# Performance work log

Hardware: AMD Instinct MI355X
Metric: run time of the kernel (lower is better)

Reference implementation:

```python
import jax, jax.numpy as jnp
import numpy as np

B, F, H, M, T = 4096, 256, 256, 3, 30
IN0 = 2 + F  # GRU layer-0 input: concat(current_pos[2], context[F])


def setup_inputs() -> dict:
    key = jax.random.key(0)
    ks = jax.random.split(key, 15)
    s = 0.05
    rn = lambda k, shp: jax.random.normal(k, shp, jnp.float32) * s
    return dict(
        context=jax.random.normal(ks[0], (B, F), jnp.float32),
        mp_w1=rn(ks[1], (64, F)), mp_b1=rn(ks[2], (64,)),
        mp_w2=rn(ks[3], (M, 64)), mp_b2=rn(ks[4], (M,)),
        w_ih0=rn(ks[5], (M, 3 * H, IN0)), w_hh0=rn(ks[6], (M, 3 * H, H)),
        b_ih0=rn(ks[7], (M, 3 * H)), b_hh0=rn(ks[8], (M, 3 * H)),
        w_ih1=rn(ks[9], (M, 3 * H, H)), w_hh1=rn(ks[10], (M, 3 * H, H)),
        b_ih1=rn(ks[11], (M, 3 * H)), b_hh1=rn(ks[12], (M, 3 * H)),
        out_w=rn(ks[13], (M, 2, H)), out_b=rn(ks[14], (M, 2)),
        num_future_steps=T,
    )


def _gru_cell(x, h, w_ih, w_hh, b_ih, b_hh):
    # PyTorch GRU cell, gate order (r, z, n)
    gx = x @ w_ih.T + b_ih  # (B, 3H)
    gh = h @ w_hh.T + b_hh  # (B, 3H)
    xr, xz, xn = jnp.split(gx, 3, axis=-1)
    hr, hz, hn = jnp.split(gh, 3, axis=-1)
    r = jax.nn.sigmoid(xr + hr)
    z = jax.nn.sigmoid(xz + hz)
    n = jnp.tanh(xn + r * hn)
    return (1.0 - z) * n + z * h


def reference(context, mp_w1, mp_b1, mp_w2, mp_b2,
              w_ih0, w_hh0, b_ih0, b_hh0,
              w_ih1, w_hh1, b_ih1, b_hh1,
              out_w, out_b, num_future_steps):
    mode_logits = jax.nn.relu(context @ mp_w1.T + mp_b1) @ mp_w2.T + mp_b2
    mode_probs = jax.nn.softmax(mode_logits, axis=-1)  # (B, M)

    def decode_mode(wi0, wh0, bi0, bh0, wi1, wh1, bi1, bh1, ow, ob):
        def step(carry, _):
            h0, h1, pos = carry
            x = jnp.concatenate([pos, context], axis=-1)  # (B, 2+F)
            h0n = _gru_cell(x, h0, wi0, wh0, bi0, bh0)
            h1n = _gru_cell(h0n, h1, wi1, wh1, bi1, bh1)
            delta = h1n @ ow.T + ob  # (B, 2)
            return (h0n, h1n, delta), delta

        pos0 = jnp.zeros((context.shape[0], 2), context.dtype)
        # hidden = context.unsqueeze(0).repeat(2,1,1): both layers init to context
        (_, _, _), deltas = jax.lax.scan(step, (context, context, pos0), None,
                                          length=num_future_steps)
        # deltas: (T, B, 2) -> (B, T, 2), cumulative sum over time
        return jnp.cumsum(deltas.transpose(1, 0, 2), axis=1)

    trajs = jax.vmap(decode_mode)(w_ih0, w_hh0, b_ih0, b_hh0,
                                  w_ih1, w_hh1, b_ih1, b_hh1,
                                  out_w, out_b)  # (M, B, T, 2)
    trajectories = trajs.transpose(1, 0, 2, 3)  # (B, M, T, 2)
    return trajectories, mode_probs
```

## Files before the change

kernel.cpp:

```cpp
#include <hip/hip_runtime.h>


typedef __attribute__((ext_vector_type(8))) short bf16x8;
typedef __attribute__((ext_vector_type(4))) float f32x4;
typedef __fp16 f16x2 __attribute__((ext_vector_type(2)));

__device__ __forceinline__ short f2bf(float f) {
    unsigned u = __builtin_bit_cast(unsigned, f);
    unsigned r = (u + 0x7fffu + ((u >> 16) & 1u)) >> 16;
    return (short)r;
}
__device__ __forceinline__ float bf2f(short s) {
    unsigned u = ((unsigned)(unsigned short)s) << 16;
    return __builtin_bit_cast(float, u);
}
__device__ __forceinline__ unsigned pkh2(float a, float b) {
    f16x2 v = __builtin_amdgcn_cvt_pkrtz(a, b);
    return __builtin_bit_cast(unsigned, v);
}
__device__ __forceinline__ float uph(unsigned u, int hi) {
    f16x2 v = __builtin_bit_cast(f16x2, u);
    return (float)(hi ? v[1] : v[0]);
}
__device__ __forceinline__ float fast_sigmoid(float x) {
    x = fminf(fmaxf(x, -30.f), 30.f);
    float e = __builtin_amdgcn_exp2f(x * -1.442695041f);
    return __builtin_amdgcn_rcpf(1.f + e);
}
__device__ __forceinline__ float fast_tanh(float x) {
    x = fminf(fmaxf(x, -15.f), 15.f);
    float e = __builtin_amdgcn_exp2f(x * -2.885390082f);
    return (1.f - e) * __builtin_amdgcn_rcpf(1.f + e);
}

__global__ void prep_kernel(const float* __restrict__ w_ih0,
                            const float* __restrict__ w_hh0,
                            const float* __restrict__ w_ih1,
                            const float* __restrict__ w_hh1,
                            short* __restrict__ ws) {
    int bid = blockIdx.x;
    int L = threadIdx.x;
    const float* src;
    int srcRowLen, colBase, m, w, ks, t;
    if (bid < 1152) {
        int idx = bid, mw = idx / 48, blk = idx % 48;
        m = mw / 8; w = mw % 8;
        if (blk < 32) { ks = blk >> 2; t = blk & 3; }
        else { int q = blk - 32; ks = q >> 1; t = 4 + (q & 1); }
        src = w_hh0 + (size_t)m * 768 * 256; srcRowLen = 256; colBase = 0;
    } else if (bid < 3456) {
        int idx = bid - 1152, mw = idx / 96, blk = idx % 96;
        m = mw / 8; w = mw % 8;
        int half;
        if (blk < 64) { half = blk >> 5; ks = (blk >> 2) & 7; t = blk & 3; }
        else { int q = blk - 64; half = q >> 4; ks = (q >> 1) & 7; t = 4 + (q & 1); }
        src = (half ? w_hh1 : w_ih1) + (size_t)m * 768 * 256;
        srcRowLen = 256; colBase = 0;
    } else {
        int idx = bid - 3456, mw = idx / 48, blk = idx % 48;
        m = mw / 8; w = mw % 8; ks = blk / 6; t = blk % 6;
        src = w_ih0 + (size_t)m * 768 * 258; srcRowLen = 258; colBase = 2;
    }
    int row = (t >> 1) * 256 + 32 * w + (t & 1) * 16 + (L & 15);
    int col0 = colBase + ks * 32 + (L >> 4) * 8;
    short* dst = ws + (size_t)bid * 512 + L * 8;
    const float* s = src + (size_t)row * srcRowLen + col0;
#pragma unroll
    for (int j = 0; j < 8; ++j) dst[j] = f2bf(s[j]);
}

__global__ __launch_bounds__(256) void modeprobs_kernel(
    const float* __restrict__ ctx, const float* __restrict__ w1,
    const float* __restrict__ b1, const float* __restrict__ w2,
    const float* __restrict__ b2, float* __restrict__ out,
    long probs_off) {
    __shared__ float w1s[64 * 256];
    int tid = threadIdx.x;
    int j = tid & 63;
    int rsub = tid >> 6;
#pragma unroll
    for (int i = 0; i < 64; ++i) w1s[tid + i * 256] = w1[tid + i * 256];
    float b1v = b1[j];
    float w2v0 = w2[j], w2v1 = w2[64 + j], w2v2 = w2[128 + j];
    float b20 = b2[0], b21 = b2[1], b22 = b2[2];
    __syncthreads();
    for (int c = 0; c < 16; ++c) {
        int brow = blockIdx.x * 64 + c * 4 + rsub;
        const float* crow = ctx + (size_t)brow * 256;
        float accv = b1v;
#pragma unroll 8
        for (int k = 0; k < 256; ++k) {
            int kk = (k + j) & 255;
            accv += w1s[j * 256 + kk] * crow[kk];
        }
        float h = fmaxf(accv, 0.f);
        float l0 = h * w2v0, l1 = h * w2v1, l2 = h * w2v2;
#pragma unroll
        for (int s = 1; s < 64; s <<= 1) {
            l0 += __shfl_xor(l0, s);
            l1 += __shfl_xor(l1, s);
            l2 += __shfl_xor(l2, s);
        }
        if (j == 0) {
            l0 += b20; l1 += b21; l2 += b22;
            float mx = fmaxf(l0, fmaxf(l1, l2));
            float e0 = __builtin_amdgcn_exp2f((l0 - mx) * 1.442695041f);
            float e1 = __builtin_amdgcn_exp2f((l1 - mx) * 1.442695041f);
            float e2 = __builtin_amdgcn_exp2f((l2 - mx) * 1.442695041f);
            float inv = 1.f / (e0 + e1 + e2);
            out[probs_off + (size_t)brow * 3 + 0] = e0 * inv;
            out[probs_off + (size_t)brow * 3 + 1] = e1 * inv;
            out[probs_off + (size_t)brow * 3 + 2] = e2 * inv;
        }
    }
}

__global__ __launch_bounds__(512, 2) void decoder_kernel(
    const float* __restrict__ context,
    const float* __restrict__ w_ih0_f,
    const float* __restrict__ b_ih0, const float* __restrict__ b_hh0,
    const float* __restrict__ b_ih1, const float* __restrict__ b_hh1,
    const float* __restrict__ out_w, const float* __restrict__ out_b,
    const short* __restrict__ ws, float* __restrict__ out,
    const int* __restrict__ pT, int ntiles) {
    __shared__ short ctxS[64 * 264];
    __shared__ short h0s[64 * 264];
    __shared__ short h1s[64 * 264];
    __shared__ float posD[128];
    __shared__ float owl[512];
    __shared__ float cwp0[768], cwp1[768];
    __shared__ float cbA[512];
    __shared__ float cbXn[256];
    __shared__ float cbh0n[256];
    __shared__ float cb1A[512];
    __shared__ float cb1X[256];
    __shared__ float cb1H[256];

    const int bid = blockIdx.x;
    const int xcd = bid & 7, slot = bid >> 3;
    int mode, xl, nx;
    if (xcd < 3)      { mode = 0; xl = xcd;     nx = 3; }
    else if (xcd < 6) { mode = 1; xl = xcd - 3; nx = 3; }
    else              { mode = 2; xl = xcd - 6; nx = 2; }
    const int g = slot * nx + xl;
    if (g >= ntiles) return;
    const int m = mode;
    const int b0 = g * 64;

    const int T = *pT;
    const int tid = threadIdx.x;
    const int lane = tid & 63, w = tid >> 6;
    const int lr = lane & 15, quad = lane >> 4;

    if (tid < 128) posD[tid] = 0.f;
    owl[tid] = out_w[m * 512 + tid];
    if (tid < 512) {
        cbA[tid] = b_ih0[m * 768 + tid] + b_hh0[m * 768 + tid];
        cb1A[tid] = b_ih1[m * 768 + tid] + b_hh1[m * 768 + tid];
    }
    if (tid < 256) {
        cbXn[tid] = b_ih0[m * 768 + 512 + tid];
        cbh0n[tid] = b_hh0[m * 768 + 512 + tid];
        cb1X[tid] = b_ih1[m * 768 + 512 + tid];
        cb1H[tid] = b_hh1[m * 768 + 512 + tid];
    }
    for (int c = tid; c < 768; c += 512) {
        cwp0[c] = w_ih0_f[((size_t)m * 768 + c) * 258 + 0];
        cwp1[c] = w_ih0_f[((size_t)m * 768 + c) * 258 + 1];
    }
#pragma unroll
    for (int i = 0; i < 32; ++i) {
        int idx = tid + i * 512;
        int r = idx >> 8, k = idx & 255;
        short v = f2bf(context[(size_t)(b0 + r) * 256 + k]);
        ctxS[r * 264 + k] = v;
        h0s[r * 264 + k] = v;
        h1s[r * 264 + k] = v;
    }
    const float ob0v = out_b[m * 2 + 0], ob1v = out_b[m * 2 + 1];

    const short* p0w = ws + ((size_t)(m * 8 + w) * 48) * 512 + lane * 8;
    const short* p1w = ws + (size_t)1152 * 512 + ((size_t)(m * 8 + w) * 96) * 512 + lane * 8;
    const short* pcw = ws + (size_t)3456 * 512 + ((size_t)(m * 8 + w) * 48) * 512 + lane * 8;

    const int cA = 32 * w + lr;
    const int cB = 32 * w + 16 + lr;

    __syncthreads();

    float cum0 = 0.f, cum1 = 0.f;

    for (int st = 0; st < T; ++st) {
        unsigned rp[2][4][2], zp[2][4][2];

        {
            f32x4 arz[4][4];
#pragma unroll
            for (int rt = 0; rt < 4; ++rt)
#pragma unroll
                for (int r = 0; r < 4; ++r) {
                    int row = rt * 16 + quad * 4 + r;
                    float px = posD[row * 2], py = posD[row * 2 + 1];
#pragma unroll
                    for (int t = 0; t < 4; ++t) {
                        int c = (t >> 1) * 256 + ((t & 1) ? cB : cA);
                        arz[t][rt][r] = cbA[c] + px * cwp0[c] + py * cwp1[c];
                    }
                }
            const short* bpc = pcw;
            const short* bp0 = p0w;
#pragma unroll 1
            for (int ks = 0; ks < 8; ++ks) {
                bf16x8 ac[4], ah[4];
#pragma unroll
                for (int rt = 0; rt < 4; ++rt) {
                    ac[rt] = *reinterpret_cast<const bf16x8*>(
                        ctxS + (rt * 16 + lr) * 264 + ks * 32 + quad * 8);
                    ah[rt] = *reinterpret_cast<const bf16x8*>(
                        h0s + (rt * 16 + lr) * 264 + ks * 32 + quad * 8);
                }
#pragma unroll
                for (int t = 0; t < 4; ++t) {
                    bf16x8 b = *reinterpret_cast<const bf16x8*>(bpc + t * 512);
#pragma unroll
                    for (int rt = 0; rt < 4; ++rt)
                        arz[t][rt] = __builtin_amdgcn_mfma_f32_16x16x32_bf16(
                            ac[rt], b, arz[t][rt], 0, 0, 0);
                }
#pragma unroll
                for (int t = 0; t < 4; ++t) {
                    bf16x8 b = *reinterpret_cast<const bf16x8*>(bp0 + t * 512);
#pragma unroll
                    for (int rt = 0; rt < 4; ++rt)
                        arz[t][rt] = __builtin_amdgcn_mfma_f32_16x16x32_bf16(
                            ah[rt], b, arz[t][rt], 0, 0, 0);
                }
                bpc += 6 * 512;
                bp0 += 4 * 512;
            }
#pragma unroll
            for (int nt = 0; nt < 2; ++nt)
#pragma unroll
                for (int rt = 0; rt < 4; ++rt) {
                    rp[nt][rt][0] = pkh2(fast_sigmoid(arz[nt][rt][0]),
                                         fast_sigmoid(arz[nt][rt][1]));
                    rp[nt][rt][1] = pkh2(fast_sigmoid(arz[nt][rt][2]),
                                         fast_sigmoid(arz[nt][rt][3]));
                    zp[nt][rt][0] = pkh2(fast_sigmoid(arz[2 + nt][rt][0]),
                                         fast_sigmoid(arz[2 + nt][rt][1]));
                    zp[nt][rt][1] = pkh2(fast_sigmoid(arz[2 + nt][rt][2]),
                                         fast_sigmoid(arz[2 + nt][rt][3]));
                }
        }
        {
            f32x4 axn[2][4], ahn[2][4];
#pragma unroll
            for (int rt = 0; rt < 4; ++rt)
#pragma unroll
                for (int r = 0; r < 4; ++r) {
                    int row = rt * 16 + quad * 4 + r;
                    float px = posD[row * 2], py = posD[row * 2 + 1];
#pragma unroll
                    for (int nt = 0; nt < 2; ++nt) {
                        int cn = nt ? cB : cA;
                        axn[nt][rt][r] = cbXn[cn] + px * cwp0[512 + cn] +
                                         py * cwp1[512 + cn];
                        ahn[nt][rt][r] = cbh0n[cn];
                    }
                }
            const short* bpc = pcw + 4 * 512;
            const short* bp0 = p0w + 32 * 512;
#pragma unroll 1
            for (int ks = 0; ks < 8; ++ks) {
                bf16x8 ac[4], ah[4];
#pragma unroll
                for (int rt = 0; rt < 4; ++rt) {
                    ac[rt] = *reinterpret_cast<const bf16x8*>(
                        ctxS + (rt * 16 + lr) * 264 + ks * 32 + quad * 8);
                    ah[rt] = *reinterpret_cast<const bf16x8*>(
                        h0s + (rt * 16 + lr) * 264 + ks * 32 + quad * 8);
                }
#pragma unroll
                for (int nt = 0; nt < 2; ++nt) {
                    bf16x8 b = *reinterpret_cast<const bf16x8*>(bpc + nt * 512);
#pragma unroll
                    for (int rt = 0; rt < 4; ++rt)
                        axn[nt][rt] = __builtin_amdgcn_mfma_f32_16x16x32_bf16(
                            ac[rt], b, axn[nt][rt], 0, 0, 0);
                }
#pragma unroll
                for (int nt = 0; nt < 2; ++nt) {
                    bf16x8 b = *reinterpret_cast<const bf16x8*>(bp0 + nt * 512);
#pragma unroll
                    for (int rt = 0; rt < 4; ++rt)
                        ahn[nt][rt] = __builtin_amdgcn_mfma_f32_16x16x32_bf16(
                            ah[rt], b, ahn[nt][rt], 0, 0, 0);
                }
                bpc += 6 * 512;
                bp0 += 2 * 512;
            }
            __syncthreads();
#pragma unroll
            for (int nt = 0; nt < 2; ++nt) {
                int col = nt ? cB : cA;
#pragma unroll
                for (int rt = 0; rt < 4; ++rt)
#pragma unroll
                    for (int r = 0; r < 4; ++r) {
                        int row = rt * 16 + quad * 4 + r;
                        float rr = uph(rp[nt][rt][r >> 1], r & 1);
                        float zz = uph(zp[nt][rt][r >> 1], r & 1);
                        float nn =
                            fast_tanh(axn[nt][rt][r] + rr * ahn[nt][rt][r]);
                        float hold = bf2f(h0s[row * 264 + col]);
                        h0s[row * 264 + col] = f2bf((1.f - zz) * nn + zz * hold);
                    }
            }
        }
        __syncthreads();

        {
            f32x4 arz[4][4];
#pragma unroll
            for (int rt = 0; rt < 4; ++rt)
#pragma unroll
                for (int r = 0; r < 4; ++r)
#pragma unroll
                    for (int t = 0; t < 4; ++t) {
                        int c = (t >> 1) * 256 + ((t & 1) ? cB : cA);
                        arz[t][rt][r] = cb1A[c];
                    }
            const short* bq0 = p1w;
            const short* bq1 = p1w + 32 * 512;
#pragma unroll 1
            for (int ks = 0; ks < 8; ++ks) {
                bf16x8 a0[4], a1[4];
#pragma unroll
                for (int rt = 0; rt < 4; ++rt) {
                    a0[rt] = *reinterpret_cast<const bf16x8*>(
                        h0s + (rt * 16 + lr) * 264 + ks * 32 + quad * 8);
                    a1[rt] = *reinterpret_cast<const bf16x8*>(
                        h1s + (rt * 16 + lr) * 264 + ks * 32 + quad * 8);
                }
#pragma unroll
                for (int t = 0; t < 4; ++t) {
                    bf16x8 b = *reinterpret_cast<const bf16x8*>(bq0 + t * 512);
#pragma unroll
                    for (int rt = 0; rt < 4; ++rt)
                        arz[t][rt] = __builtin_amdgcn_mfma_f32_16x16x32_bf16(
                            a0[rt], b, arz[t][rt], 0, 0, 0);
                }
#pragma unroll
                for (int t = 0; t < 4; ++t) {
                    bf16x8 b = *reinterpret_cast<const bf16x8*>(bq1 + t * 512);
#pragma unroll
                    for (int rt = 0; rt < 4; ++rt)
                        arz[t][rt] = __builtin_amdgcn_mfma_f32_16x16x32_bf16(
                            a1[rt], b, arz[t][rt], 0, 0, 0);
                }
                bq0 += 4 * 512;
                bq1 += 4 * 512;
            }
#pragma unroll
            for (int nt = 0; nt < 2; ++nt)
#pragma unroll
                for (int rt = 0; rt < 4; ++rt) {
                    rp[nt][rt][0] = pkh2(fast_sigmoid(arz[nt][rt][0]),
                                         fast_sigmoid(arz[nt][rt][1]));
                    rp[nt][rt][1] = pkh2(fast_sigmoid(arz[nt][rt][2]),
                                         fast_sigmoid(arz[nt][rt][3]));
                    zp[nt][rt][0] = pkh2(fast_sigmoid(arz[2 + nt][rt][0]),
                                         fast_sigmoid(arz[2 + nt][rt][1]));
                    zp[nt][rt][1] = pkh2(fast_sigmoid(arz[2 + nt][rt][2]),
                                         fast_sigmoid(arz[2 + nt][rt][3]));
                }
        }
        {
            f32x4 axn[2][4], ahn[2][4];
#pragma unroll
            for (int rt = 0; rt < 4; ++rt)
#pragma unroll
                for (int r = 0; r < 4; ++r)
#pragma unroll
                    for (int nt = 0; nt < 2; ++nt) {
                        int cn = nt ? cB : cA;
                        axn[nt][rt][r] = cb1X[cn];
                        ahn[nt][rt][r] = cb1H[cn];
                    }
            const short* bx = p1w + 64 * 512;
            const short* bh = p1w + 80 * 512;
#pragma unroll 1
            for (int ks = 0; ks < 8; ++ks) {
                bf16x8 a0[4], a1[4];
#pragma unroll
                for (int rt = 0; rt < 4; ++rt) {
                    a0[rt] = *reinterpret_cast<const bf16x8*>(
                        h0s + (rt * 16 + lr) * 264 + ks * 32 + quad * 8);
                    a1[rt] = *reinterpret_cast<const bf16x8*>(
                        h1s + (rt * 16 + lr) * 264 + ks * 32 + quad * 8);
                }
#pragma unroll
                for (int nt = 0; nt < 2; ++nt) {
                    bf16x8 b = *reinterpret_cast<const bf16x8*>(bx + nt * 512);
#pragma unroll
                    for (int rt = 0; rt < 4; ++rt)
                        axn[nt][rt] = __builtin_amdgcn_mfma_f32_16x16x32_bf16(
                            a0[rt], b, axn[nt][rt], 0, 0, 0);
                }
#pragma unroll
                for (int nt = 0; nt < 2; ++nt) {
                    bf16x8 b = *reinterpret_cast<const bf16x8*>(bh + nt * 512);
#pragma unroll
                    for (int rt = 0; rt < 4; ++rt)
                        ahn[nt][rt] = __builtin_amdgcn_mfma_f32_16x16x32_bf16(
                            a1[rt], b, ahn[nt][rt], 0, 0, 0);
                }
                bx += 2 * 512;
                bh += 2 * 512;
            }
            __syncthreads();
#pragma unroll
            for (int nt = 0; nt < 2; ++nt) {
                int col = nt ? cB : cA;
#pragma unroll
                for (int rt = 0; rt < 4; ++rt)
#pragma unroll
                    for (int r = 0; r < 4; ++r) {
                        int row = rt * 16 + quad * 4 + r;
                        float rr = uph(rp[nt][rt][r >> 1], r & 1);
                        float zz = uph(zp[nt][rt][r >> 1], r & 1);
                        float nn =
                            fast_tanh(axn[nt][rt][r] + rr * ahn[nt][rt][r]);
                        float hold = bf2f(h1s[row * 264 + col]);
                        h1s[row * 264 + col] = f2bf((1.f - zz) * nn + zz * hold);
                    }
            }
        }
        __syncthreads();

        {
            int brow = tid >> 3, p = tid & 7;
            float d0 = 0.f, d1 = 0.f;
#pragma unroll
            for (int j = 0; j < 4; ++j) {
                int cb = ((p + brow) & 7) * 8 + j * 64;
                bf16x8 hv8 = *reinterpret_cast<const bf16x8*>(h1s + brow * 264 + cb);
#pragma unroll
                for (int i = 0; i < 8; ++i) {
                    float hv = bf2f(hv8[i]);
                    d0 += hv * owl[cb + i];
                    d1 += hv * owl[256 + cb + i];
                }
            }
            d0 += __shfl_xor(d0, 1); d0 += __shfl_xor(d0, 2); d0 += __shfl_xor(d0, 4);
            d1 += __shfl_xor(d1, 1); d1 += __shfl_xor(d1, 2); d1 += __shfl_xor(d1, 4);
            d0 += ob0v;
            d1 += ob1v;
            if (p == 0) {
                cum0 += d0;
                cum1 += d1;
                size_t o = (((size_t)(b0 + brow) * 3 + m) * (size_t)T + st) * 2;
                out[o] = cum0;
                out[o + 1] = cum1;
                posD[brow * 2] = d0;
                posD[brow * 2 + 1] = d1;
            }
        }
        __syncthreads();
    }
}

extern "C" void kernel_launch(void* const* d_in, const int* in_sizes, int n_in,
                              void* d_out, int out_size, void* d_ws, size_t ws_size,
                              hipStream_t stream) {
    const float* context = (const float*)d_in[0];
    const float* mp_w1 = (const float*)d_in[1];
    const float* mp_b1 = (const float*)d_in[2];
    const float* mp_w2 = (const float*)d_in[3];
    const float* mp_b2 = (const float*)d_in[4];
    const float* w_ih0 = (const float*)d_in[5];
    const float* w_hh0 = (const float*)d_in[6];
    const float* b_ih0 = (const float*)d_in[7];
    const float* b_hh0 = (const float*)d_in[8];
    const float* w_ih1 = (const float*)d_in[9];
    const float* w_hh1 = (const float*)d_in[10];
    const float* b_ih1 = (const float*)d_in[11];
    const float* b_hh1 = (const float*)d_in[12];
    const float* out_w = (const float*)d_in[13];
    const float* out_b = (const float*)d_in[14];
    const int* pT = (const int*)d_in[15];
    float* out = (float*)d_out;
    short* ws = (short*)d_ws;

    const int B = in_sizes[0] / 256;
    const int ntiles = B / 64;
    const long probs_off = (long)out_size - (long)B * 3;

    prep_kernel<<<4608, 64, 0, stream>>>(w_ih0, w_hh0, w_ih1, w_hh1, ws);
    modeprobs_kernel<<<B / 64, 256, 0, stream>>>(context, mp_w1, mp_b1, mp_w2,
                                                 mp_b2, out, probs_off);
    const int nslots = (ntiles + 1) / 2;
    decoder_kernel<<<8 * nslots, 512, 0, stream>>>(
        context, w_ih0, b_ih0, b_hh0, b_ih1, b_hh1, out_w, out_b, ws, out, pT,
        ntiles);
}
```

Measured before the change: 1.045 ms.

## Hoist time-invariant context projection out of GRU step loop into AGPRs

The layer-0 input projection of the constant context (W_ih0 times context plus biases) is now computed once before the time loop and stored as packed bf16 in accumulator registers. Each step reads it back instead of redoing the context MFMAs, which removes about 40% of layer-0 matrix work per step and the ctxS shared buffer. The cost is extra register pressure from 48 AGPRs, which may hurt occupancy under the 512x2 launch bounds. Rounding the precomputed projection to bf16 also adds some precision loss.

```diff
diff --git a/kernel.cpp b/kernel.cpp
--- a/kernel.cpp
+++ b/kernel.cpp
@@ -14,6 +14,12 @@
     unsigned u = ((unsigned)(unsigned short)s) << 16;
     return __builtin_bit_cast(float, u);
 }
+__device__ __forceinline__ unsigned pk2(float a, float b) {
+    return (unsigned)(unsigned short)f2bf(a) | ((unsigned)(unsigned short)f2bf(b) << 16);
+}
+__device__ __forceinline__ float unpk(unsigned u, int hi) {
+    return __builtin_bit_cast(float, hi ? (u & 0xffff0000u) : (u << 16));
+}
 __device__ __forceinline__ unsigned pkh2(float a, float b) {
     f16x2 v = __builtin_amdgcn_cvt_pkrtz(a, b);
     return __builtin_bit_cast(unsigned, v);
@@ -31,6 +37,14 @@
     x = fminf(fmaxf(x, -15.f), 15.f);
     float e = __builtin_amdgcn_exp2f(x * -2.885390082f);
     return (1.f - e) * __builtin_amdgcn_rcpf(1.f + e);
+}
+__device__ __forceinline__ void aw(unsigned& dst, unsigned v) {
+    asm volatile("v_accvgpr_write_b32 %0, %1" : "=a"(dst) : "v"(v));
+}
+__device__ __forceinline__ unsigned ar(unsigned a) {
+    unsigned v;
+    asm("v_accvgpr_read_b32 %0, %1" : "=v"(v) : "a"(a));
+    return v;
 }
 
 __global__ void prep_kernel(const float* __restrict__ w_ih0,
@@ -123,14 +137,11 @@
     const float* __restrict__ out_w, const float* __restrict__ out_b,
     const short* __restrict__ ws, float* __restrict__ out,
     const int* __restrict__ pT, int ntiles) {
-    __shared__ short ctxS[64 * 264];
     __shared__ short h0s[64 * 264];
     __shared__ short h1s[64 * 264];
     __shared__ float posD[128];
     __shared__ float owl[512];
     __shared__ float cwp0[768], cwp1[768];
-    __shared__ float cbA[512];
-    __shared__ float cbXn[256];
     __shared__ float cbh0n[256];
     __shared__ float cb1A[512];
     __shared__ float cb1X[256];
@@ -154,12 +165,8 @@
 
     if (tid < 128) posD[tid] = 0.f;
     owl[tid] = out_w[m * 512 + tid];
-    if (tid < 512) {
-        cbA[tid] = b_ih0[m * 768 + tid] + b_hh0[m * 768 + tid];
-        cb1A[tid] = b_ih1[m * 768 + tid] + b_hh1[m * 768 + tid];
-    }
+    if (tid < 512) cb1A[tid] = b_ih1[m * 768 + tid] + b_hh1[m * 768 + tid];
     if (tid < 256) {
-        cbXn[tid] = b_ih0[m * 768 + 512 + tid];
         cbh0n[tid] = b_hh0[m * 768 + 512 + tid];
         cb1X[tid] = b_ih1[m * 768 + 512 + tid];
         cb1H[tid] = b_hh1[m * 768 + 512 + tid];
@@ -173,7 +180,6 @@
         int idx = tid + i * 512;
         int r = idx >> 8, k = idx & 255;
         short v = f2bf(context[(size_t)(b0 + r) * 256 + k]);
-        ctxS[r * 264 + k] = v;
         h0s[r * 264 + k] = v;
         h1s[r * 264 + k] = v;
     }
@@ -188,6 +194,43 @@
 
     __syncthreads();
 
+    unsigned gx[48];
+    {
+        f32x4 acc[6][4];
+#pragma unroll
+        for (int t6 = 0; t6 < 6; ++t6) {
+            int c = (t6 >> 1) * 256 + 32 * w + (t6 & 1) * 16 + lr;
+            float bi = b_ih0[m * 768 + c] + (t6 < 4 ? b_hh0[m * 768 + c] : 0.f);
+#pragma unroll
+            for (int rt = 0; rt < 4; ++rt) acc[t6][rt] = f32x4{bi, bi, bi, bi};
+        }
+        const short* bp = pcw;
+#pragma unroll 1
+        for (int ks = 0; ks < 8; ++ks) {
+            bf16x8 a[4];
+#pragma unroll
+            for (int rt = 0; rt < 4; ++rt)
+                a[rt] = *reinterpret_cast<const bf16x8*>(
+                    h0s + (rt * 16 + lr) * 264 + ks * 32 + quad * 8);
+#pragma unroll
+            for (int t6 = 0; t6 < 6; ++t6) {
+                bf16x8 b = *reinterpret_cast<const bf16x8*>(bp + t6 * 512);
+#pragma unroll
+                for (int rt = 0; rt < 4; ++rt)
+                    acc[t6][rt] = __builtin_amdgcn_mfma_f32_16x16x32_bf16(
+                        a[rt], b, acc[t6][rt], 0, 0, 0);
+            }
+            bp += 6 * 512;
+        }
+#pragma unroll
+        for (int t6 = 0; t6 < 6; ++t6)
+#pragma unroll
+            for (int rt = 0; rt < 4; ++rt) {
+                aw(gx[(t6 * 4 + rt) * 2 + 0], pk2(acc[t6][rt][0], acc[t6][rt][1]));
+                aw(gx[(t6 * 4 + rt) * 2 + 1], pk2(acc[t6][rt][2], acc[t6][rt][3]));
+            }
+    }
+
     float cum0 = 0.f, cum1 = 0.f;
 
     for (int st = 0; st < T; ++st) {
@@ -204,29 +247,19 @@
 #pragma unroll
                     for (int t = 0; t < 4; ++t) {
                         int c = (t >> 1) * 256 + ((t & 1) ? cB : cA);
-                        arz[t][rt][r] = cbA[c] + px * cwp0[c] + py * cwp1[c];
+                        arz[t][rt][r] =
+                            unpk(ar(gx[(t * 4 + rt) * 2 + (r >> 1)]), r & 1) +
+                            px * cwp0[c] + py * cwp1[c];
                     }
                 }
-            const short* bpc = pcw;
             const short* bp0 = p0w;
 #pragma unroll 1
             for (int ks = 0; ks < 8; ++ks) {
-                bf16x8 ac[4], ah[4];
-#pragma unroll
-                for (int rt = 0; rt < 4; ++rt) {
-                    ac[rt] = *reinterpret_cast<const bf16x8*>(
-                        ctxS + (rt * 16 + lr) * 264 + ks * 32 + quad * 8);
+                bf16x8 ah[4];
+#pragma unroll
+                for (int rt = 0; rt < 4; ++rt)
                     ah[rt] = *reinterpret_cast<const bf16x8*>(
                         h0s + (rt * 16 + lr) * 264 + ks * 32 + quad * 8);
-                }
-#pragma unroll
-                for (int t = 0; t < 4; ++t) {
-                    bf16x8 b = *reinterpret_cast<const bf16x8*>(bpc + t * 512);
-#pragma unroll
-                    for (int rt = 0; rt < 4; ++rt)
-                        arz[t][rt] = __builtin_amdgcn_mfma_f32_16x16x32_bf16(
-                            ac[rt], b, arz[t][rt], 0, 0, 0);
-                }
 #pragma unroll
                 for (int t = 0; t < 4; ++t) {
                     bf16x8 b = *reinterpret_cast<const bf16x8*>(bp0 + t * 512);
@@ -235,7 +268,6 @@
                         arz[t][rt] = __builtin_amdgcn_mfma_f32_16x16x32_bf16(
                             ah[rt], b, arz[t][rt], 0, 0, 0);
                 }
-                bpc += 6 * 512;
                 bp0 += 4 * 512;
             }
 #pragma unroll
@@ -253,41 +285,22 @@
                 }
         }
         {
-            f32x4 axn[2][4], ahn[2][4];
+            f32x4 ahn[2][4];
 #pragma unroll
             for (int rt = 0; rt < 4; ++rt)
 #pragma unroll
-                for (int r = 0; r < 4; ++r) {
-                    int row = rt * 16 + quad * 4 + r;
-                    float px = posD[row * 2], py = posD[row * 2 + 1];
-#pragma unroll
-                    for (int nt = 0; nt < 2; ++nt) {
-                        int cn = nt ? cB : cA;
-                        axn[nt][rt][r] = cbXn[cn] + px * cwp0[512 + cn] +
-                                         py * cwp1[512 + cn];
-                        ahn[nt][rt][r] = cbh0n[cn];
-                    }
-                }
-            const short* bpc = pcw + 4 * 512;
+                for (int r = 0; r < 4; ++r)
+#pragma unroll
+                    for (int nt = 0; nt < 2; ++nt)
+                        ahn[nt][rt][r] = cbh0n[nt ? cB : cA];
             const short* bp0 = p0w + 32 * 512;
 #pragma unroll 1
             for (int ks = 0; ks < 8; ++ks) {
-                bf16x8 ac[4], ah[4];
-#pragma unroll
-                for (int rt = 0; rt < 4; ++rt) {
-                    ac[rt] = *reinterpret_cast<const bf16x8*>(
-                        ctxS + (rt * 16 + lr) * 264 + ks * 32 + quad * 8);
+                bf16x8 ah[4];
+#pragma unroll
+                for (int rt = 0; rt < 4; ++rt)
                     ah[rt] = *reinterpret_cast<const bf16x8*>(
                         h0s + (rt * 16 + lr) * 264 + ks * 32 + quad * 8);
-                }
-#pragma unroll
-                for (int nt = 0; nt < 2; ++nt) {
-                    bf16x8 b = *reinterpret_cast<const bf16x8*>(bpc + nt * 512);
-#pragma unroll
-                    for (int rt = 0; rt < 4; ++rt)
-                        axn[nt][rt] = __builtin_amdgcn_mfma_f32_16x16x32_bf16(
-                            ac[rt], b, axn[nt][rt], 0, 0, 0);
-                }
 #pragma unroll
                 for (int nt = 0; nt < 2; ++nt) {
                     bf16x8 b = *reinterpret_cast<const bf16x8*>(bp0 + nt * 512);
@@ -296,7 +309,6 @@
                         ahn[nt][rt] = __builtin_amdgcn_mfma_f32_16x16x32_bf16(
                             ah[rt], b, ahn[nt][rt], 0, 0, 0);
                 }
-                bpc += 6 * 512;
                 bp0 += 2 * 512;
             }
             __syncthreads();
@@ -308,10 +320,13 @@
 #pragma unroll
                     for (int r = 0; r < 4; ++r) {
                         int row = rt * 16 + quad * 4 + r;
+                        float px = posD[row * 2], py = posD[row * 2 + 1];
                         float rr = uph(rp[nt][rt][r >> 1], r & 1);
                         float zz = uph(zp[nt][rt][r >> 1], r & 1);
-                        float nn =
-                            fast_tanh(axn[nt][rt][r] + rr * ahn[nt][rt][r]);
+                        float xn =
+                            unpk(ar(gx[((4 + nt) * 4 + rt) * 2 + (r >> 1)]), r & 1) +
+                            px * cwp0[512 + col] + py * cwp1[512 + col];
+                        float nn = fast_tanh(xn + rr * ahn[nt][rt][r]);
                         float hold = bf2f(h0s[row * 264 + col]);
                         h0s[row * 264 + col] = f2bf((1.f - zz) * nn + zz * hold);
                     }
```

Result: slower. 1.647 ms (+57.7%).
